# Optimization experiments

Hardware: AMD Instinct MI355X
Metric: run time of the kernel (lower is better)

The kernel has to match this reference:

```python
import jax, jax.numpy as jnp
import numpy as np

H = 32  # hidden size, fixed by the source module


def setup_inputs() -> dict:
    key = jax.random.key(0)
    ks = jax.random.split(key, 11)
    B, T = 1024, 999
    s = 0.1  # weight init scale
    return {
        "input": jax.random.normal(ks[0], (B, T), jnp.float32),
        "W_ih1": jax.random.normal(ks[1], (4 * H, 1), jnp.float32) * s,
        "W_hh1": jax.random.normal(ks[2], (4 * H, H), jnp.float32) * s,
        "b_ih1": jax.random.normal(ks[3], (4 * H,), jnp.float32) * s,
        "b_hh1": jax.random.normal(ks[4], (4 * H,), jnp.float32) * s,
        "W_ih2": jax.random.normal(ks[5], (4 * H, H), jnp.float32) * s,
        "W_hh2": jax.random.normal(ks[6], (4 * H, H), jnp.float32) * s,
        "b_ih2": jax.random.normal(ks[7], (4 * H,), jnp.float32) * s,
        "b_hh2": jax.random.normal(ks[8], (4 * H,), jnp.float32) * s,
        "W_lin": jax.random.normal(ks[9], (1, H), jnp.float32) * s,
        "b_lin": jax.random.normal(ks[10], (1,), jnp.float32) * s,
        "future": 1000,
    }


def _lstm_cell(x, h, c, W_ih, W_hh, b_ih, b_hh):
    # PyTorch LSTMCell: gates = x@W_ih^T + b_ih + h@W_hh^T + b_hh, order i,f,g,o
    z = x @ W_ih.T + h @ W_hh.T + (b_ih + b_hh)
    i, f, g, o = jnp.split(z, 4, axis=-1)
    c_new = jax.nn.sigmoid(f) * c + jax.nn.sigmoid(i) * jnp.tanh(g)
    h_new = jax.nn.sigmoid(o) * jnp.tanh(c_new)
    return h_new, c_new


def reference(input, W_ih1, W_hh1, b_ih1, b_hh1, W_ih2, W_hh2, b_ih2, b_hh2,
              W_lin, b_lin, future):
    B = input.shape[0]
    dt = input.dtype
    z = jnp.zeros((B, H), dt)

    def step_tf(carry, x_t):  # teacher-forced phase, x_t: [B]
        h1, c1, h2, c2 = carry
        h1, c1 = _lstm_cell(x_t[:, None], h1, c1, W_ih1, W_hh1, b_ih1, b_hh1)
        h2, c2 = _lstm_cell(h1, h2, c2, W_ih2, W_hh2, b_ih2, b_hh2)
        out = h2 @ W_lin.T + b_lin  # [B,1]
        return (h1, c1, h2, c2), out[:, 0]

    carry, outs1 = jax.lax.scan(step_tf, (z, z, z, z), input.T)  # outs1: [T,B]

    def step_gen(carry, _):
        h1, c1, h2, c2, out = carry
        h1, c1 = _lstm_cell(out, h1, c1, W_ih1, W_hh1, b_ih1, b_hh1)
        h2, c2 = _lstm_cell(h1, h2, c2, W_ih2, W_hh2, b_ih2, b_hh2)
        out = h2 @ W_lin.T + b_lin
        return (h1, c1, h2, c2, out), out[:, 0]

    last_out = outs1[-1][:, None]
    _, outs2 = jax.lax.scan(step_gen, (*carry, last_out), None, length=future)

    return jnp.concatenate([outs1, outs2], axis=0).T  # [B, T+future]
```

## Files before the change

### kernel.cpp

```cpp
#include <hip/hip_runtime.h>

#define HH 32
#define LOG2E 1.44269504088896340736f
#define KCH 32

typedef float v2f __attribute__((ext_vector_type(2)));

#define SWZ(v, pat) __int_as_float(__builtin_amdgcn_ds_swizzle(__float_as_int(v), (pat)))

__device__ __forceinline__ float hw_exp2(float x) {
    float r; asm("v_exp_f32 %0, %1" : "=v"(r) : "v"(x)); return r;
}
__device__ __forceinline__ float sigm_e(float z, float e) {
    return __builtin_amdgcn_rcpf(1.0f + hw_exp2(z * e));
}
__device__ __forceinline__ v2f pk_fma(v2f a, v2f b, v2f c) {
    return __builtin_elementwise_fma(a, b, c);
}
__device__ __forceinline__ void load_bc(const float* p, v2f* d) {
#pragma unroll
    for (int r = 0; r < 8; ++r) {
        float4 v = ((const float4*)p)[r];
        d[2*r]   = (v2f){v.x, v.y};
        d[2*r+1] = (v2f){v.z, v.w};
    }
}


__global__ __launch_bounds__(128, 2)
void lstm_seq_kernel(const float* __restrict__ input,
                     const float* __restrict__ W_ih1, const float* __restrict__ W_hh1,
                     const float* __restrict__ b_ih1, const float* __restrict__ b_hh1,
                     const float* __restrict__ W_ih2, const float* __restrict__ W_hh2,
                     const float* __restrict__ b_ih2, const float* __restrict__ b_hh2,
                     const float* __restrict__ W_lin, const float* __restrict__ b_lin,
                     float* __restrict__ out, int T, int total)
{
    const int b    = blockIdx.x;
    const int tid  = threadIdx.x;
    const int w    = tid >> 6;
    const int lane = tid & 63;
    const int ch   = lane & 31;
    const int rowA = lane;
    const int rowB = lane + 64;
    const bool lo  = lane < HH;

    __shared__ __align__(16) float ring[2 * KCH * HH];
    __shared__ __align__(16) float h1x[HH];
    __shared__ __align__(16) float h2s[HH];
    __shared__ float xbuf;

    const float esB = lo ? (-2.0f * LOG2E) : (-LOG2E);
    const float mB  = lo ? 2.0f : 1.0f;
    const float cB  = lo ? -1.0f : 0.0f;

    v2f m1A[16], m1B[16], m2A[16], m2B[16];
    float wxA = 0.f, wxB = 0.f, bA = 0.f, bB = 0.f, wl = 0.f, blin = 0.f;
    if (w == 0) {
        const v2f* pA = (const v2f*)(W_hh1 + rowA * HH);
        const v2f* pB = (const v2f*)(W_hh1 + rowB * HH);
#pragma unroll
        for (int r = 0; r < 16; ++r) { m1A[r] = pA[r]; m1B[r] = pB[r]; }
        wxA = W_ih1[rowA]; wxB = W_ih1[rowB];
        bA  = b_ih1[rowA] + b_hh1[rowA];
        bB  = b_ih1[rowB] + b_hh1[rowB];
    } else {
        const v2f* pA = (const v2f*)(W_ih2 + rowA * HH);
        const v2f* pB = (const v2f*)(W_ih2 + rowB * HH);
        const v2f* qA = (const v2f*)(W_hh2 + rowA * HH);
        const v2f* qB = (const v2f*)(W_hh2 + rowB * HH);
#pragma unroll
        for (int r = 0; r < 16; ++r) { m1A[r] = pA[r]; m1B[r] = pB[r];
                                       m2A[r] = qA[r]; m2B[r] = qB[r]; }
        bA  = b_ih2[rowA] + b_hh2[rowA];
        bB  = b_ih2[rowB] + b_hh2[rowB];
        wl  = W_lin[ch]; blin = b_lin[0];
    }

    float cst = 0.0f;
    v2f aA0 = {0.f,0.f}, aA1 = {0.f,0.f}, aB0 = {0.f,0.f}, aB1 = {0.f,0.f};
    v2f eA0 = {0.f,0.f}, eA1 = {0.f,0.f}, eB0 = {0.f,0.f}, eB1 = {0.f,0.f};
    v2f h2v[16];
#pragma unroll
    for (int r = 0; r < 16; ++r) h2v[r] = (v2f){0.f, 0.f};

    const float* __restrict__ inp  = input + (size_t)b * T;
    float* __restrict__       outp = out   + (size_t)b * total;

    if (w == 0) {
        int t = 0;
        for (int c = 0; t < T; ++c) {
            float* buf = ring + (c & 1) * (KCH * HH);
            int S = T - t; if (S > KCH) S = KCH;
            for (int s = 0; s < S; ++s, ++t) {
                float x   = inp[t];
                float z1A = fmaf(x, wxA, bA + (aA0.x + aA0.y) + (aA1.x + aA1.y));
                float z1B = fmaf(x, wxB, bB + (aB0.x + aB0.y) + (aB1.x + aB1.y));
                float actA = sigm_e(z1A, -LOG2E);
                float actB = fmaf(mB, sigm_e(z1B, esB), cB);
                float fG = __shfl_xor(actA, 32, 64);
                float oG = __shfl_xor(actB, 32, 64);
                cst = fmaf(fG, cst, actA * actB);
                float h1 = oG * fmaf(2.0f, sigm_e(cst, -2.0f * LOG2E), -1.0f);
                float* slot = buf + s * HH;
                if (lo) slot[lane] = h1;
                v2f h1v[16]; load_bc(slot, h1v);
                aA0 = (v2f){0.f,0.f}; aA1 = (v2f){0.f,0.f};
                aB0 = (v2f){0.f,0.f}; aB1 = (v2f){0.f,0.f};
#pragma unroll
                for (int r = 0; r < 16; r += 2) {
                    aA0 = pk_fma(h1v[r],   m1A[r],   aA0);
                    aA1 = pk_fma(h1v[r+1], m1A[r+1], aA1);
                    aB0 = pk_fma(h1v[r],   m1B[r],   aB0);
                    aB1 = pk_fma(h1v[r+1], m1B[r+1], aB1);
                }
            }
            __syncthreads();
        }
        __syncthreads();
    } else {
        __syncthreads();
        int t = 0;
        for (int c = 0; t < T; ++c) {
            const float* buf = ring + (c & 1) * (KCH * HH);
            int S = T - t; if (S > KCH) S = KCH;
            for (int s = 0; s < S; ++s, ++t) {
                v2f h1v[16]; load_bc(buf + s * HH, h1v);
                v2f sA0 = eA0, sA1 = eA1, sB0 = eB0, sB1 = eB1;
#pragma unroll
                for (int r = 0; r < 16; r += 2) {
                    sA0 = pk_fma(h1v[r],   m1A[r],   sA0);
                    sA1 = pk_fma(h1v[r+1], m1A[r+1], sA1);
                    sB0 = pk_fma(h1v[r],   m1B[r],   sB0);
                    sB1 = pk_fma(h1v[r+1], m1B[r+1], sB1);
                }
                float z2A = bA + (sA0.x + sA0.y) + (sA1.x + sA1.y);
                float z2B = bB + (sB0.x + sB0.y) + (sB1.x + sB1.y);
                float actA = sigm_e(z2A, -LOG2E);
                float actB = fmaf(mB, sigm_e(z2B, esB), cB);
                float fG = __shfl_xor(actA, 32, 64);
                float oG = __shfl_xor(actB, 32, 64);
                cst = fmaf(fG, cst, actA * actB);
                float h2 = oG * fmaf(2.0f, sigm_e(cst, -2.0f * LOG2E), -1.0f);
                float p = h2 * wl;
                p += SWZ(p, 0x041F); p += SWZ(p, 0x081F); p += SWZ(p, 0x101F);
                p += SWZ(p, 0x201F); p += SWZ(p, 0x401F);
                float ov = p + blin;
                if (lane == 0) { outp[t] = ov; xbuf = ov; }
                if (lo) h2s[lane] = h2;
                load_bc(h2s, h2v);
                eA0 = (v2f){0.f,0.f}; eA1 = (v2f){0.f,0.f};
                eB0 = (v2f){0.f,0.f}; eB1 = (v2f){0.f,0.f};
#pragma unroll
                for (int r = 0; r < 16; r += 2) {
                    eA0 = pk_fma(h2v[r],   m2A[r],   eA0);
                    eA1 = pk_fma(h2v[r+1], m2A[r+1], eA1);
                    eB0 = pk_fma(h2v[r],   m2B[r],   eB0);
                    eB1 = pk_fma(h2v[r+1], m2B[r+1], eB1);
                }
            }
            __syncthreads();
        }
    }

    for (int t = T; t < total; ++t) {
        __syncthreads();
        if (w == 0) {
            float x   = xbuf;
            float z1A = fmaf(x, wxA, bA + (aA0.x + aA0.y) + (aA1.x + aA1.y));
            float z1B = fmaf(x, wxB, bB + (aB0.x + aB0.y) + (aB1.x + aB1.y));
            float actA = sigm_e(z1A, -LOG2E);
            float actB = fmaf(mB, sigm_e(z1B, esB), cB);
            float fG = __shfl_xor(actA, 32, 64);
            float oG = __shfl_xor(actB, 32, 64);
            cst = fmaf(fG, cst, actA * actB);
            float h1 = oG * fmaf(2.0f, sigm_e(cst, -2.0f * LOG2E), -1.0f);
            if (lo) h1x[lane] = h1;
        } else {
            eA0 = (v2f){0.f,0.f}; eA1 = (v2f){0.f,0.f};
            eB0 = (v2f){0.f,0.f}; eB1 = (v2f){0.f,0.f};
#pragma unroll
            for (int r = 0; r < 16; r += 2) {
                eA0 = pk_fma(h2v[r],   m2A[r],   eA0);
                eA1 = pk_fma(h2v[r+1], m2A[r+1], eA1);
                eB0 = pk_fma(h2v[r],   m2B[r],   eB0);
                eB1 = pk_fma(h2v[r+1], m2B[r+1], eB1);
            }
        }
        __syncthreads();
        if (w == 0) {
            v2f h1v[16]; load_bc(h1x, h1v);
            aA0 = (v2f){0.f,0.f}; aA1 = (v2f){0.f,0.f};
            aB0 = (v2f){0.f,0.f}; aB1 = (v2f){0.f,0.f};
#pragma unroll
            for (int r = 0; r < 16; r += 2) {
                aA0 = pk_fma(h1v[r],   m1A[r],   aA0);
                aA1 = pk_fma(h1v[r+1], m1A[r+1], aA1);
                aB0 = pk_fma(h1v[r],   m1B[r],   aB0);
                aB1 = pk_fma(h1v[r+1], m1B[r+1], aB1);
            }
        } else {
            v2f h1v[16]; load_bc(h1x, h1v);
            v2f sA0 = eA0, sA1 = eA1, sB0 = eB0, sB1 = eB1;
#pragma unroll
            for (int r = 0; r < 16; r += 2) {
                sA0 = pk_fma(h1v[r],   m1A[r],   sA0);
                sA1 = pk_fma(h1v[r+1], m1A[r+1], sA1);
                sB0 = pk_fma(h1v[r],   m1B[r],   sB0);
                sB1 = pk_fma(h1v[r+1], m1B[r+1], sB1);
            }
            float z2A = bA + (sA0.x + sA0.y) + (sA1.x + sA1.y);
            float z2B = bB + (sB0.x + sB0.y) + (sB1.x + sB1.y);
            float actA = sigm_e(z2A, -LOG2E);
            float actB = fmaf(mB, sigm_e(z2B, esB), cB);
            float fG = __shfl_xor(actA, 32, 64);
            float oG = __shfl_xor(actB, 32, 64);
            cst = fmaf(fG, cst, actA * actB);
            float h2 = oG * fmaf(2.0f, sigm_e(cst, -2.0f * LOG2E), -1.0f);
            float p = h2 * wl;
            p += SWZ(p, 0x041F); p += SWZ(p, 0x081F); p += SWZ(p, 0x101F);
            p += SWZ(p, 0x201F); p += SWZ(p, 0x401F);
            float ov = p + blin;
            if (lane == 0) { outp[t] = ov; xbuf = ov; }
            if (lo) h2s[lane] = h2;
            load_bc(h2s, h2v);
        }
    }
}

extern "C" void kernel_launch(void* const* d_in, const int* in_sizes, int n_in,
                              void* d_out, int out_size, void* d_ws, size_t ws_size,
                              hipStream_t stream) {
    const int B = 1024;
    const int T = in_sizes[0] / B;
    const int total = out_size / B;

    lstm_seq_kernel<<<dim3(B), dim3(128), 0, stream>>>(
        (const float*)d_in[0],
        (const float*)d_in[1], (const float*)d_in[2],
        (const float*)d_in[3], (const float*)d_in[4],
        (const float*)d_in[5], (const float*)d_in[6],
        (const float*)d_in[7], (const float*)d_in[8],
        (const float*)d_in[9], (const float*)d_in[10],
        (float*)d_out, T, total);
}
```

Baseline: 1.315 ms.

## Interleave LSTM gate rows per quad and exchange gates with DPP broadcasts

Reassigns gate rows so each group of four lanes holds the i,f,g,o rows of one hidden unit, which lets gates be exchanged through quad-perm DPP instead of cross-half shuffles. Each lane now updates two cell states. The output projection reduction switches to DPP rotations plus fewer swizzles, and the h2 recurrence matvec moves back into the same step. The next input is prefetched one step ahead and the ring chunk size is halved. This trades a little extra per-lane activation work and more frequent barriers for shorter dependent latency on the serial path.

After: 1.209 ms. 8.0% less time.

```diff
diff --git a/kernel.cpp b/kernel.cpp
--- a/kernel.cpp
+++ b/kernel.cpp
@@ -2,10 +2,18 @@
 
 #define HH 32
 #define LOG2E 1.44269504088896340736f
-#define KCH 32
+#define KCH 16
 
 typedef float v2f __attribute__((ext_vector_type(2)));
 
+#define DPPF(v, ctrl) \
+    __int_as_float(__builtin_amdgcn_update_dpp(0, __float_as_int(v), (ctrl), 0xF, 0xF, true))
+#define QP_B0 0x00
+#define QP_B1 0x55
+#define QP_B2 0xAA
+#define QP_B3 0xFF
+#define DPP_ROR4  0x124
+#define DPP_ROR8  0x128
 #define SWZ(v, pat) __int_as_float(__builtin_amdgcn_ds_swizzle(__float_as_int(v), (pat)))
 
 __device__ __forceinline__ float hw_exp2(float x) {
@@ -25,7 +33,13 @@
         d[2*r+1] = (v2f){v.z, v.w};
     }
 }
-
+__device__ __forceinline__ float out_reduce(float p) {
+    p += DPPF(p, DPP_ROR4);
+    p += DPPF(p, DPP_ROR8);
+    p += SWZ(p, 0x401F);
+    p += __shfl_xor(p, 32, 64);
+    return p;
+}
 
 __global__ __launch_bounds__(128, 2)
 void lstm_seq_kernel(const float* __restrict__ input,
@@ -40,22 +54,23 @@
     const int tid  = threadIdx.x;
     const int w    = tid >> 6;
     const int lane = tid & 63;
-    const int ch   = lane & 31;
-    const int rowA = lane;
-    const int rowB = lane + 64;
-    const bool lo  = lane < HH;
+    const int q    = lane & 3;
+    const int ch   = lane >> 2;
+    const int rowA = (q << 5) | ch;
+    const int rowB = (q << 5) | (ch + 16);
 
     __shared__ __align__(16) float ring[2 * KCH * HH];
     __shared__ __align__(16) float h1x[HH];
     __shared__ __align__(16) float h2s[HH];
     __shared__ float xbuf;
 
-    const float esB = lo ? (-2.0f * LOG2E) : (-LOG2E);
-    const float mB  = lo ? 2.0f : 1.0f;
-    const float cB  = lo ? -1.0f : 0.0f;
+    const bool  isg = (q == 2);
+    const float es  = isg ? (-2.0f * LOG2E) : (-LOG2E);
+    const float mm  = isg ? 2.0f : 1.0f;
+    const float cc  = isg ? -1.0f : 0.0f;
 
     v2f m1A[16], m1B[16], m2A[16], m2B[16];
-    float wxA = 0.f, wxB = 0.f, bA = 0.f, bB = 0.f, wl = 0.f, blin = 0.f;
+    float wxA = 0.f, wxB = 0.f, bA, bB, wlA = 0.f, wlB = 0.f, blin = 0.f;
     if (w == 0) {
         const v2f* pA = (const v2f*)(W_hh1 + rowA * HH);
         const v2f* pB = (const v2f*)(W_hh1 + rowB * HH);
@@ -74,45 +89,48 @@
                                        m2A[r] = qA[r]; m2B[r] = qB[r]; }
         bA  = b_ih2[rowA] + b_hh2[rowA];
         bB  = b_ih2[rowB] + b_hh2[rowB];
-        wl  = W_lin[ch]; blin = b_lin[0];
-    }
-
-    float cst = 0.0f;
-    v2f aA0 = {0.f,0.f}, aA1 = {0.f,0.f}, aB0 = {0.f,0.f}, aB1 = {0.f,0.f};
-    v2f eA0 = {0.f,0.f}, eA1 = {0.f,0.f}, eB0 = {0.f,0.f}, eB1 = {0.f,0.f};
-    v2f h2v[16];
-#pragma unroll
-    for (int r = 0; r < 16; ++r) h2v[r] = (v2f){0.f, 0.f};
+        wlA = W_lin[ch]; wlB = W_lin[ch + 16]; blin = b_lin[0];
+    }
+
+    float cA = 0.f, cB = 0.f;
+    v2f p0 = {0.f,0.f}, p1 = {0.f,0.f}, p2 = {0.f,0.f}, p3 = {0.f,0.f};
 
     const float* __restrict__ inp  = input + (size_t)b * T;
     float* __restrict__       outp = out   + (size_t)b * total;
 
     if (w == 0) {
         int t = 0;
-        for (int c = 0; t < T; ++c) {
-            float* buf = ring + (c & 1) * (KCH * HH);
+        float xcur = inp[0];
+        for (int cb = 0; t < T; ++cb) {
+            float* buf = ring + (cb & 1) * (KCH * HH);
             int S = T - t; if (S > KCH) S = KCH;
             for (int s = 0; s < S; ++s, ++t) {
-                float x   = inp[t];
-                float z1A = fmaf(x, wxA, bA + (aA0.x + aA0.y) + (aA1.x + aA1.y));
-                float z1B = fmaf(x, wxB, bB + (aB0.x + aB0.y) + (aB1.x + aB1.y));
-                float actA = sigm_e(z1A, -LOG2E);
-                float actB = fmaf(mB, sigm_e(z1B, esB), cB);
-                float fG = __shfl_xor(actA, 32, 64);
-                float oG = __shfl_xor(actB, 32, 64);
-                cst = fmaf(fG, cst, actA * actB);
-                float h1 = oG * fmaf(2.0f, sigm_e(cst, -2.0f * LOG2E), -1.0f);
+                float x = xcur;
+                int tn = t + 1;
+                xcur = inp[tn < T ? tn : 0];
+                float z1A = fmaf(x, wxA, bA + (p0.x + p0.y) + (p1.x + p1.y));
+                float z1B = fmaf(x, wxB, bB + (p2.x + p2.y) + (p3.x + p3.y));
+                float acA = fmaf(mm, sigm_e(z1A, es), cc);
+                float acB = fmaf(mm, sigm_e(z1B, es), cc);
+                float iA = DPPF(acA, QP_B0), fA = DPPF(acA, QP_B1);
+                float gA = DPPF(acA, QP_B2), oA = DPPF(acA, QP_B3);
+                float iB = DPPF(acB, QP_B0), fB = DPPF(acB, QP_B1);
+                float gB = DPPF(acB, QP_B2), oB = DPPF(acB, QP_B3);
+                cA = fmaf(fA, cA, iA * gA);
+                cB = fmaf(fB, cB, iB * gB);
+                float hA = oA * fmaf(2.0f, sigm_e(cA, -2.0f * LOG2E), -1.0f);
+                float hB = oB * fmaf(2.0f, sigm_e(cB, -2.0f * LOG2E), -1.0f);
                 float* slot = buf + s * HH;
-                if (lo) slot[lane] = h1;
-                v2f h1v[16]; load_bc(slot, h1v);
-                aA0 = (v2f){0.f,0.f}; aA1 = (v2f){0.f,0.f};
-                aB0 = (v2f){0.f,0.f}; aB1 = (v2f){0.f,0.f};
+                if (q == 0) { slot[ch] = hA; slot[ch + 16] = hB; }
+                v2f hv[16]; load_bc(slot, hv);
+                p0 = (v2f){0.f,0.f}; p1 = (v2f){0.f,0.f};
+                p2 = (v2f){0.f,0.f}; p3 = (v2f){0.f,0.f};
 #pragma unroll
                 for (int r = 0; r < 16; r += 2) {
-                    aA0 = pk_fma(h1v[r],   m1A[r],   aA0);
-                    aA1 = pk_fma(h1v[r+1], m1A[r+1], aA1);
-                    aB0 = pk_fma(h1v[r],   m1B[r],   aB0);
-                    aB1 = pk_fma(h1v[r+1], m1B[r+1], aB1);
+                    p0 = pk_fma(hv[r],   m1A[r],   p0);
+                    p1 = pk_fma(hv[r+1], m1A[r+1], p1);
+                    p2 = pk_fma(hv[r],   m1B[r],   p2);
+                    p3 = pk_fma(hv[r+1], m1B[r+1], p3);
                 }
             }
             __syncthreads();
@@ -121,43 +139,45 @@
     } else {
         __syncthreads();
         int t = 0;
-        for (int c = 0; t < T; ++c) {
-            const float* buf = ring + (c & 1) * (KCH * HH);
+        for (int cb = 0; t < T; ++cb) {
+            const float* buf = ring + (cb & 1) * (KCH * HH);
             int S = T - t; if (S > KCH) S = KCH;
             for (int s = 0; s < S; ++s, ++t) {
-                v2f h1v[16]; load_bc(buf + s * HH, h1v);
-                v2f sA0 = eA0, sA1 = eA1, sB0 = eB0, sB1 = eB1;
+                v2f hv[16]; load_bc(buf + s * HH, hv);
+                v2f s0 = p0, s1 = p1, s2 = p2, s3 = p3;
 #pragma unroll
                 for (int r = 0; r < 16; r += 2) {
-                    sA0 = pk_fma(h1v[r],   m1A[r],   sA0);
-                    sA1 = pk_fma(h1v[r+1], m1A[r+1], sA1);
-                    sB0 = pk_fma(h1v[r],   m1B[r],   sB0);
-                    sB1 = pk_fma(h1v[r+1], m1B[r+1], sB1);
+                    s0 = pk_fma(hv[r],   m1A[r],   s0);
+                    s1 = pk_fma(hv[r+1], m1A[r+1], s1);
+                    s2 = pk_fma(hv[r],   m1B[r],   s2);
+                    s3 = pk_fma(hv[r+1], m1B[r+1], s3);
                 }
-                float z2A = bA + (sA0.x + sA0.y) + (sA1.x + sA1.y);
-                float z2B = bB + (sB0.x + sB0.y) + (sB1.x + sB1.y);
-                float actA = sigm_e(z2A, -LOG2E);
-                float actB = fmaf(mB, sigm_e(z2B, esB), cB);
-                float fG = __shfl_xor(actA, 32, 64);
-                float oG = __shfl_xor(actB, 32, 64);
-                cst = fmaf(fG, cst, actA * actB);
-                float h2 = oG * fmaf(2.0f, sigm_e(cst, -2.0f * LOG2E), -1.0f);
-                float p = h2 * wl;
-                p += SWZ(p, 0x041F); p += SWZ(p, 0x081F); p += SWZ(p, 0x101F);
-                p += SWZ(p, 0x201F); p += SWZ(p, 0x401F);
-                float ov = p + blin;
+                float z2A = bA + (s0.x + s0.y) + (s1.x + s1.y);
+                float z2B = bB + (s2.x + s2.y) + (s3.x + s3.y);
+                float acA = fmaf(mm, sigm_e(z2A, es), cc);
+                float acB = fmaf(mm, sigm_e(z2B, es), cc);
+                float iA = DPPF(acA, QP_B0), fA = DPPF(acA, QP_B1);
+                float gA = DPPF(acA, QP_B2), oA = DPPF(acA, QP_B3);
+                float iB = DPPF(acB, QP_B0), fB = DPPF(acB, QP_B1);
+                float gB = DPPF(acB, QP_B2), oB = DPPF(acB, QP_B3);
+                cA = fmaf(fA, cA, iA * gA);
+                cB = fmaf(fB, cB, iB * gB);
+                float hA = oA * fmaf(2.0f, sigm_e(cA, -2.0f * LOG2E), -1.0f);
+                float hB = oB * fmaf(2.0f, sigm_e(cB, -2.0f * LOG2E), -1.0f);
+                if (q == 0) { h2s[ch] = hA; h2s[ch + 16] = hB; }
+                v2f gv[16]; load_bc(h2s, gv);
+                p0 = (v2f){0.f,0.f}; p1 = (v2f){0.f,0.f};
+                p2 = (v2f){0.f,0.f}; p3 = (v2f){0.f,0.f};
+#pragma unroll
+                for (int r = 0; r < 16; r += 2) {
+                    p0 = pk_fma(gv[r],   m2A[r],   p0);
+                    p1 = pk_fma(gv[r+1], m2A[r+1], p1);
+                    p2 = pk_fma(gv[r],   m2B[r],   p2);
+                    p3 = pk_fma(gv[r+1], m2B[r+1], p3);
+                }
+                float pr = fmaf(hA, wlA, hB * wlB);
+                float ov = out_reduce(pr) + blin;
                 if (lane == 0) { outp[t] = ov; xbuf = ov; }
-                if (lo) h2s[lane] = h2;
-                load_bc(h2s, h2v);
-                eA0 = (v2f){0.f,0.f}; eA1 = (v2f){0.f,0.f};
-                eB0 = (v2f){0.f,0.f}; eB1 = (v2f){0.f,0.f};
-#pragma unroll
-                for (int r = 0; r < 16; r += 2) {
-                    eA0 = pk_fma(h2v[r],   m2A[r],   eA0);
-                    eA1 = pk_fma(h2v[r+1], m2A[r+1], eA1);
-                    eB0 = pk_fma(h2v[r],   m2B[r],   eB0);
-                    eB1 = pk_fma(h2v[r+1], m2B[r+1], eB1);
-                }
             }
             __syncthreads();
         }
@@ -166,64 +186,70 @@
     for (int t = T; t < total; ++t) {
         __syncthreads();
         if (w == 0) {
-            float x   = xbuf;
-            float z1A = fmaf(x, wxA, bA + (aA0.x + aA0.y) + (aA1.x + aA1.y));
-            float z1B = fmaf(x, wxB, bB + (aB0.x + aB0.y) + (aB1.x + aB1.y));
-            float actA = sigm_e(z1A, -LOG2E);
-            float actB = fmaf(mB, sigm_e(z1B, esB), cB);
-            float fG = __shfl_xor(actA, 32, 64);
-            float oG = __shfl_xor(actB, 32, 64);
-            cst = fmaf(fG, cst, actA * actB);
-            float h1 = oG * fmaf(2.0f, sigm_e(cst, -2.0f * LOG2E), -1.0f);
-            if (lo) h1x[lane] = h1;
+            float x = xbuf;
+            float z1A = fmaf(x, wxA, bA + (p0.x + p0.y) + (p1.x + p1.y));
+            float z1B = fmaf(x, wxB, bB + (p2.x + p2.y) + (p3.x + p3.y));
+            float acA = fmaf(mm, sigm_e(z1A, es), cc);
+            float acB = fmaf(mm, sigm_e(z1B, es), cc);
+            float iA = DPPF(acA, QP_B0), fA = DPPF(acA, QP_B1);
+            float gA = DPPF(acA, QP_B2), oA = DPPF(acA, QP_B3);
+            float iB = DPPF(acB, QP_B0), fB = DPPF(acB, QP_B1);
+            float gB = DPPF(acB, QP_B2), oB = DPPF(acB, QP_B3);
+            cA = fmaf(fA, cA, iA * gA);
+            cB = fmaf(fB, cB, iB * gB);
+            float hA = oA * fmaf(2.0f, sigm_e(cA, -2.0f * LOG2E), -1.0f);
+            float hB = oB * fmaf(2.0f, sigm_e(cB, -2.0f * LOG2E), -1.0f);
+            if (q == 0) { h1x[ch] = hA; h1x[ch + 16] = hB; }
         } else {
-            eA0 = (v2f){0.f,0.f}; eA1 = (v2f){0.f,0.f};
-            eB0 = (v2f){0.f,0.f}; eB1 = (v2f){0.f,0.f};
+            v2f gv[16]; load_bc(h2s, gv);
+            p0 = (v2f){0.f,0.f}; p1 = (v2f){0.f,0.f};
+            p2 = (v2f){0.f,0.f}; p3 = (v2f){0.f,0.f};
 #pragma unroll
             for (int r = 0; r < 16; r += 2) {
-                eA0 = pk_fma(h2v[r],   m2A[r],   eA0);
-                eA1 = pk_fma(h2v[r+1], m2A[r+1], eA1);
-                eB0 = pk_fma(h2v[r],   m2B[r],   eB0);
-                eB1 = pk_fma(h2v[r+1], m2B[r+1], eB1);
+                p0 = pk_fma(gv[r],   m2A[r],   p0);
+                p1 = pk_fma(gv[r+1], m2A[r+1], p1);
+                p2 = pk_fma(gv[r],   m2B[r],   p2);
+                p3 = pk_fma(gv[r+1], m2B[r+1], p3);
             }
         }
         __syncthreads();
         if (w == 0) {
-            v2f h1v[16]; load_bc(h1x, h1v);
-            aA0 = (v2f){0.f,0.f}; aA1 = (v2f){0.f,0.f};
-            aB0 = (v2f){0.f,0.f}; aB1 = (v2f){0.f,0.f};
+            v2f hv[16]; load_bc(h1x, hv);
+            p0 = (v2f){0.f,0.f}; p1 = (v2f){0.f,0.f};
+            p2 = (v2f){0.f,0.f}; p3 = (v2f){0.f,0.f};
 #pragma unroll
             for (int r = 0; r < 16; r += 2) {
-                aA0 = pk_fma(h1v[r],   m1A[r],   aA0);
-                aA1 = pk_fma(h1v[r+1], m1A[r+1], aA1);
-                aB0 = pk_fma(h1v[r],   m1B[r],   aB0);
-                aB1 = pk_fma(h1v[r+1], m1B[r+1], aB1);
+                p0 = pk_fma(hv[r],   m1A[r],   p0);
+                p1 = pk_fma(hv[r+1], m1A[r+1], p1);
+                p2 = pk_fma(hv[r],   m1B[r],   p2);
+                p3 = pk_fma(hv[r+1], m1B[r+1], p3);
             }
         } else {
-            v2f h1v[16]; load_bc(h1x, h1v);
-            v2f sA0 = eA0, sA1 = eA1, sB0 = eB0, sB1 = eB1;
+            v2f hv[16]; load_bc(h1x, hv);
+            v2f s0 = p0, s1 = p1, s2 = p2, s3 = p3;
 #pragma unroll
             for (int r = 0; r < 16; r += 2) {
-                sA0 = pk_fma(h1v[r],   m1A[r],   sA0);
-                sA1 = pk_fma(h1v[r+1], m1A[r+1], sA1);
-                sB0 = pk_fma(h1v[r],   m1B[r],   sB0);
-                sB1 = pk_fma(h1v[r+1], m1B[r+1], sB1);
-            }
-            float z2A = bA + (sA0.x + sA0.y) + (sA1.x + sA1.y);
-            float z2B = bB + (sB0.x + sB0.y) + (sB1.x + sB1.y);
-            float actA = sigm_e(z2A, -LOG2E);
-            float actB = fmaf(mB, sigm_e(z2B, esB), cB);
-            float fG = __shfl_xor(actA, 32, 64);
-            float oG = __shfl_xor(actB, 32, 64);
-            cst = fmaf(fG, cst, actA * actB);
-            float h2 = oG * fmaf(2.0f, sigm_e(cst, -2.0f * LOG2E), -1.0f);
-            float p = h2 * wl;
-            p += SWZ(p, 0x041F); p += SWZ(p, 0x081F); p += SWZ(p, 0x101F);
-            p += SWZ(p, 0x201F); p += SWZ(p, 0x401F);
-            float ov = p + blin;
+                s0 = pk_fma(hv[r],   m1A[r],   s0);
+                s1 = pk_fma(hv[r+1], m1A[r+1], s1);
+                s2 = pk_fma(hv[r],   m1B[r],   s2);
+                s3 = pk_fma(hv[r+1], m1B[r+1], s3);
+            }
+            float z2A = bA + (s0.x + s0.y) + (s1.x + s1.y);
+            float z2B = bB + (s2.x + s2.y) + (s3.x + s3.y);
+            float acA = fmaf(mm, sigm_e(z2A, es), cc);
+            float acB = fmaf(mm, sigm_e(z2B, es), cc);
+            float iA = DPPF(acA, QP_B0), fA = DPPF(acA, QP_B1);
+            float gA = DPPF(acA, QP_B2), oA = DPPF(acA, QP_B3);
+            float iB = DPPF(acB, QP_B0), fB = DPPF(acB, QP_B1);
+            float gB = DPPF(acB, QP_B2), oB = DPPF(acB, QP_B3);
+            cA = fmaf(fA, cA, iA * gA);
+            cB = fmaf(fB, cB, iB * gB);
+            float hA = oA * fmaf(2.0f, sigm_e(cA, -2.0f * LOG2E), -1.0f);
+            float hB = oB * fmaf(2.0f, sigm_e(cB, -2.0f * LOG2E), -1.0f);
+            if (q == 0) { h2s[ch] = hA; h2s[ch + 16] = hB; }
+            float pr = fmaf(hA, wlA, hB * wlB);
+            float ov = out_reduce(pr) + blin;
             if (lane == 0) { outp[t] = ov; xbuf = ov; }
-            if (lo) h2s[lane] = h2;
-            load_bc(h2s, h2v);
         }
     }
 }
```
